# Kernel optimization log

Measured on AMD Instinct MI355X. Metric: run time of the kernel, lower is better.

The kernel has to match this reference:

```python
import jax, jax.numpy as jnp
import numpy as np

T_, N_, DIN, D, HEADS, WW, E_, DPE = 8, 20000, 128, 128, 4, 4, 320000, 8
DH = D // HEADS
NEG = -1e30
EPS_GATE = 1e-6


def setup_inputs() -> dict:
    key = jax.random.key(0)
    ks = jax.random.split(key, 10)
    return {
        "H_tilde": jax.random.normal(ks[0], (T_, N_, DIN), jnp.float32),
        "S": jax.random.uniform(ks[1], (T_, N_), jnp.float32),
        "Wq": jax.random.normal(ks[2], (D, DIN), jnp.float32) * 0.05,
        "Wkh": jax.random.normal(ks[3], (D, DIN), jnp.float32) * 0.05,
        "Wkpe": jax.random.normal(ks[4], (D, DPE), jnp.float32) * 0.05,
        "Wv": jax.random.normal(ks[5], (D, DIN), jnp.float32) * 0.05,
        "pe_table": jax.random.normal(ks[6], (WW + 1, DPE), jnp.float32),
        "rel_bias": jax.random.normal(ks[7], (WW + 1,), jnp.float32),
        "src": jax.random.randint(ks[8], (E_,), 0, N_),
        "dst": jax.random.randint(ks[9], (E_,), 0, N_),
    }


def reference(H_tilde, S, Wq, Wkh, Wkpe, Wv, pe_table, rel_bias, src, dst):
    T, N, _ = H_tilde.shape
    H, dh, W = HEADS, DH, WW
    scale = dh ** -0.5
    dtype = H_tilde.dtype

    # Projections (torch Linear: x @ W.T). W_k over concat([H, pe]) splits additively.
    Q = (H_tilde @ Wq.T).reshape(T, N, H, dh)
    K0 = (H_tilde @ Wkh.T).reshape(T, N, H, dh)
    V = (H_tilde @ Wv.T).reshape(T, N, H, dh)
    pe_k = (pe_table @ Wkpe.T).reshape(W + 1, H, dh)
    gate = jnp.log(jnp.clip(S, 0.0, 1.0) + EPS_GATE)  # (T, N)

    # Pad W zero-steps in front so a length-(W+1) slice at t covers t-W..t.
    pad = lambda x: jnp.concatenate([jnp.zeros((W,) + x.shape[1:], x.dtype), x], axis=0)
    Kp, Vp, gp = pad(K0), pad(V), pad(gate)

    def step(_, tq):
        t, Qt = tq  # Qt: (N, H, dh)
        Kwin = jax.lax.dynamic_slice_in_dim(Kp, t, W + 1, 0)[::-1]  # (W+1,N,H,dh), dt=0..W
        Vwin = jax.lax.dynamic_slice_in_dim(Vp, t, W + 1, 0)[::-1]
        gwin = jax.lax.dynamic_slice_in_dim(gp, t, W + 1, 0)[::-1]  # (W+1, N)
        Qd = Qt[dst]  # (E, H, dh)

        scores = []
        for dt in range(W + 1):
            Ks = Kwin[dt][src] + pe_k[dt][None]  # (E, H, dh)
            s = (jnp.einsum('ehc,ehc->eh', Qd, Ks) * scale
                 + rel_bias[dt] + gwin[dt][src][:, None])
            scores.append(jnp.where(dt <= t, s, NEG))  # mask dt > t (W_eff = min(W, t))
        sc = jnp.stack(scores)  # (W+1, E, H)

        # Segment softmax over incoming edges of each dst node, jointly over dt.
        mx = jax.ops.segment_max(sc.transpose(1, 0, 2), dst, num_segments=N)  # (N,W+1,H)
        mx = mx.max(axis=1)  # (N, H)
        valid = (jnp.arange(W + 1) <= t)[:, None, None]
        ex = jnp.where(valid, jnp.exp(sc - mx[dst][None]), 0.0)  # (W+1, E, H)

        denom = jax.ops.segment_sum(ex.sum(axis=0), dst, num_segments=N)  # (N, H)
        numer = jnp.zeros((N, H, dh), dtype)
        for dt in range(W + 1):
            contrib = ex[dt][:, :, None] * Vwin[dt][src]  # (E, H, dh)
            numer = numer + jax.ops.segment_sum(contrib, dst, num_segments=N)

        msg = numer / jnp.maximum(denom, 1e-12)[:, :, None]  # (N, H, dh)
        return None, msg.reshape(N, H * dh)

    _, M_out = jax.lax.scan(step, None, (jnp.arange(T), Q))
    return M_out  # (T, N, d)
```

## Files before the change

kernel.cpp:

```cpp
#include <hip/hip_runtime.h>

typedef unsigned short u16;
typedef unsigned int u32;
typedef __attribute__((ext_vector_type(8))) __bf16 bf16x8;
typedef __attribute__((ext_vector_type(4))) float f32x4;
typedef __attribute__((ext_vector_type(4))) _Float16 f16x4;
typedef __attribute__((ext_vector_type(2))) unsigned u32x2;

constexpr int TT = 8, NN = 20000, DD = 128, EE = 320000;
constexpr int MAXDEG = 64;
constexpr float SCL = 0.17677669529663687f;
constexpr int VBLK2 = 544;

__device__ __forceinline__ u16 f2bf(float f) {
  return __builtin_bit_cast(u16, (__bf16)f);
}
__device__ __forceinline__ u16 f2h(float f) {
  return __builtin_bit_cast(u16, (_Float16)f);
}
__device__ __forceinline__ float blo(u32 u) { return __uint_as_float(u << 16); }
__device__ __forceinline__ float bhi(u32 u) { return __uint_as_float(u & 0xffff0000u); }

__device__ __forceinline__ bf16x8 cvt8(float4 f0, float4 f1) {
  bf16x8 r;
  r[0] = (__bf16)f0.x; r[1] = (__bf16)f0.y; r[2] = (__bf16)f0.z; r[3] = (__bf16)f0.w;
  r[4] = (__bf16)f1.x; r[5] = (__bf16)f1.y; r[6] = (__bf16)f1.z; r[7] = (__bf16)f1.w;
  return r;
}

__global__ void k_init(const float* __restrict__ pe_table, const float* __restrict__ Wkpe,
                       const float* __restrict__ Wq, const float* __restrict__ Wkh,
                       const float* __restrict__ Wv, const float* __restrict__ S,
                       float* __restrict__ pek, int* __restrict__ cnt,
                       u16* __restrict__ Wb, float* __restrict__ SgT) {
  int i = blockIdx.x * 256 + threadIdx.x;
  if (i < NN) cnt[i] = 0;
  if (i < 5 * DD) {
    int dt = i >> 7, j = i & 127;
    float s = 0.f;
    for (int p = 0; p < 8; ++p) s += pe_table[dt * 8 + p] * Wkpe[j * 8 + p];
    pek[i] = s;
  }
  if (i < 3 * DD * DD) {
    int y = i / (DD * DD), idx = i % (DD * DD);
    const float* W = (y == 0) ? Wq : (y == 1) ? Wkh : Wv;
    Wb[i] = f2bf(W[idx]);
  }
  if (i < TT * NN) {
    SgT[i] = fminf(fmaxf(S[i], 0.f), 1.f) + 1e-6f;
  }
}

__global__ void k_build(const int* __restrict__ src, const int* __restrict__ dst,
                        int* __restrict__ cnt, int* __restrict__ eslot) {
  int i = blockIdx.x * 256 + threadIdx.x;
  if (i < EE) {
    int d = dst[i];
    int p = atomicAdd(&cnt[d], 1);
    if (p < MAXDEG) eslot[d * MAXDEG + p] = src[i];
  }
}

__global__ __launch_bounds__(256) void k_proj6(
    const float* __restrict__ Hm, const u16* __restrict__ Wb,
    u16* __restrict__ Qb, u16* __restrict__ Kb, u16* __restrict__ Vb) {
  int tid = threadIdx.x;
  int lane = tid & 63, wv = tid >> 6;
  int wr = wv >> 1, wc = wv & 1;
  int l15 = lane & 15, lq = lane >> 4;
  size_t m0 = (size_t)blockIdx.x * 128;

  bf16x8 a[4][4];
#pragma unroll
  for (int ks = 0; ks < 4; ++ks) {
    int col0 = ks * 32 + lq * 8;
#pragma unroll
    for (int i = 0; i < 4; ++i) {
      const float* gp = Hm + (m0 + wr * 64 + i * 16 + l15) * DD + col0;
      a[ks][i] = cvt8(*(const float4*)gp, *(const float4*)(gp + 4));
    }
  }

  for (int y = 0; y < 3; ++y) {
    u16* Out = (y == 0) ? Qb : (y == 1) ? Kb : Vb;
    const bool asF16 = (y == 2);
    const u16* Wy = Wb + y * DD * DD;

    f32x4 acc[4][4];
    for (int i = 0; i < 4; ++i)
      for (int j = 0; j < 4; ++j) acc[i][j] = (f32x4){0.f, 0.f, 0.f, 0.f};

    for (int ks = 0; ks < 4; ++ks) {
      int col0 = ks * 32 + lq * 8;
      bf16x8 b[4];
#pragma unroll
      for (int j = 0; j < 4; ++j)
        b[j] = *(const bf16x8*)(Wy + (wc * 64 + j * 16 + l15) * DD + col0);
#pragma unroll
      for (int i = 0; i < 4; ++i)
#pragma unroll
        for (int j = 0; j < 4; ++j)
          acc[i][j] = __builtin_amdgcn_mfma_f32_16x16x32_bf16(a[ks][i], b[j], acc[i][j], 0, 0, 0);
    }

#pragma unroll
    for (int i = 0; i < 4; ++i)
#pragma unroll
      for (int j = 0; j < 4; ++j)
#pragma unroll
        for (int g = 0; g < 4; ++g) {
          size_t row = m0 + wr * 64 + i * 16 + lq * 4 + g;
          int col = wc * 64 + j * 16 + l15;
          Out[row * DD + col] = asF16 ? f2h(acc[i][j][g]) : f2bf(acc[i][j][g]);
        }
  }
}

__global__ __launch_bounds__(256, 8) void k_agg10(
    const u16* __restrict__ Qb, const u16* __restrict__ Kb, const u16* __restrict__ Vb,
    const float* __restrict__ SgT, const float* __restrict__ pek,
    const float* __restrict__ relb,
    const int* __restrict__ cnt, const int* __restrict__ eslot,
    float* __restrict__ outp) {
  __shared__ int srcS[MAXDEG];
  __shared__ float eS2[4][40];
  __shared__ u16 VldsS[4][VBLK2];
  int tid = threadIdx.x;
  const int h = tid >> 6, lane = tid & 63;
  const int n = blockIdx.x;

  int deg = min(cnt[n], MAXDEG);
  if (tid < MAXDEG) srcS[tid] = (tid < deg) ? eslot[n * MAXDEG + tid] : 0;

  const int t16 = lane & 15, qo = lane >> 4, qo4 = qo * 4;
  const int h32 = h * 32;

  uint4 qb;
  {
    bool qok = t16 < 8;
    const u16* Qp = Qb + ((size_t)(t16 & 7) * NN + n) * DD + h32 + qo * 8;
    qb = qok ? *(const uint4*)(Qp) : make_uint4(0u, 0u, 0u, 0u);
  }

  {
    float qf0 = blo(qb.x), qf1 = bhi(qb.x), qf2 = blo(qb.y), qf3 = bhi(qb.y);
    float qf4 = blo(qb.z), qf5 = bhi(qb.z), qf6 = blo(qb.w), qf7 = bhi(qb.w);
#pragma unroll
    for (int d = 0; d < 5; ++d) {
      const float* pp = pek + d * DD + h32 + qo * 8;
      float4 p0 = *(const float4*)pp;
      float4 p1 = *(const float4*)(pp + 4);
      float s = qf0 * p0.x + qf1 * p0.y + qf2 * p0.z + qf3 * p0.w
              + qf4 * p1.x + qf5 * p1.y + qf6 * p1.z + qf7 * p1.w;
      s += __shfl_xor(s, 16);
      s += __shfl_xor(s, 32);
      if (qo == 0 && t16 < 8) eS2[h][t16 * 5 + d] = __expf(s * SCL + relb[d]);
    }
  }
  __syncthreads();

  f32x4 num0 = (f32x4){0.f, 0.f, 0.f, 0.f};
  f32x4 num1 = (f32x4){0.f, 0.f, 0.f, 0.f};
  float dd = 0.f;

  if (deg > 0) {
    const int degm1 = deg - 1;
    const int nch = (deg + 15) >> 4;
    const int cmax = nch << 4;
    const int nj = nch * 8;

    const int vkey = lane >> 2, vcb = lane & 3;
    u16* vbuf = &VldsS[h][0];
    unsigned trbase = (unsigned)(uintptr_t)vbuf + lane * 8;
    unsigned woff = (unsigned)((vcb >> 1) * VBLK2 + (vkey >> 2) * 128 +
                               (vkey & 3) * 32 + (vcb & 1) * 16);

    auto loadK = [&](int tp, int c16) -> uint4 {
      return *(const uint4*)(Kb + (size_t)tp * (NN * DD)
                             + (size_t)srcS[min(c16 + t16, degm1)] * DD + h32 + qo * 8);
    };
    auto loadV = [&](int tp, int c16) -> uint4 {
      return *(const uint4*)(Vb + (size_t)tp * (NN * DD)
                             + (size_t)srcS[min(c16 + vkey, degm1)] * DD + h32 + vcb * 8);
    };
    auto loadSg = [&](int tp, int c16) -> float {
      return SgT[(size_t)tp * NN + srcS[min(c16 + t16, degm1)]];
    };
    auto writeV = [&](uint4 f) { *(uint4*)((char*)vbuf + woff) = f; };
    auto compute = [&](uint4 ka, float sg, int tp, int c16) {
      int dt = t16 - tp;
      bool tval = (dt >= 0) && (dt <= 4) && (t16 < 8);
      float Ef = tval ? eS2[h][t16 * 5 + dt] : 0.f;

      f32x4 z = (f32x4){0.f, 0.f, 0.f, 0.f};
      f32x4 sc = __builtin_amdgcn_mfma_f32_16x16x32_bf16(
          __builtin_bit_cast(bf16x8, ka), __builtin_bit_cast(bf16x8, qb), z, 0, 0, 0);

      f16x4 wf;
      float w0, w1, w2, w3;
      {
        float g0 = __shfl(sg, qo4 + 0), g1 = __shfl(sg, qo4 + 1);
        float g2 = __shfl(sg, qo4 + 2), g3 = __shfl(sg, qo4 + 3);
        g0 = ((c16 + qo4 + 0) < deg) ? g0 : 0.f;
        g1 = ((c16 + qo4 + 1) < deg) ? g1 : 0.f;
        g2 = ((c16 + qo4 + 2) < deg) ? g2 : 0.f;
        g3 = ((c16 + qo4 + 3) < deg) ? g3 : 0.f;
        w0 = __expf(sc[0] * SCL) * Ef * g0;
        w1 = __expf(sc[1] * SCL) * Ef * g1;
        w2 = __expf(sc[2] * SCL) * Ef * g2;
        w3 = __expf(sc[3] * SCL) * Ef * g3;
      }
      dd += w0 + w1 + w2 + w3;
      wf[0] = (_Float16)w0; wf[1] = (_Float16)w1;
      wf[2] = (_Float16)w2; wf[3] = (_Float16)w3;

      __builtin_amdgcn_sched_barrier(0);
      u32x2 vr0, vr1;
      asm volatile("ds_read_b64_tr_b16 %0, %1" : "=v"(vr0) : "v"(trbase));
      asm volatile("ds_read_b64_tr_b16 %0, %1 offset:544" : "=v"(vr1) : "v"(trbase));
      asm volatile("s_waitcnt lgkmcnt(0)");
      __builtin_amdgcn_sched_barrier(0);
      num0 = __builtin_amdgcn_mfma_f32_16x16x16f16(
          wf, __builtin_bit_cast(f16x4, vr0), num0, 0, 0, 0);
      num1 = __builtin_amdgcn_mfma_f32_16x16x16f16(
          wf, __builtin_bit_cast(f16x4, vr1), num1, 0, 0, 0);
    };

    uint4 kA = loadK(0, 0);
    float sgA = loadSg(0, 0);
    writeV(loadV(0, 0));
    int tpj = 0, cj = 0;
    int tpn = 0, cn = 16;
    if (cn >= cmax) { cn = 0; tpn = 1; }

    for (int j = 0; j < nj; ++j) {
      bool more = (j + 1) < nj;
      uint4 kB = make_uint4(0u, 0u, 0u, 0u), vB = make_uint4(0u, 0u, 0u, 0u);
      float sgB = 0.f;
      if (more) {
        kB = loadK(tpn, cn);
        vB = loadV(tpn, cn);
        sgB = loadSg(tpn, cn);
      }
      compute(kA, sgA, tpj, cj);
      __builtin_amdgcn_sched_barrier(0);
      if (more) writeV(vB);
      kA = kB;
      sgA = sgB;
      tpj = tpn; cj = cn;
      cn += 16;
      if (cn >= cmax) { cn = 0; ++tpn; }
    }
  }

  float Dh = dd;
  Dh += __shfl_xor(Dh, 16);
  Dh += __shfl_xor(Dh, 32);
#pragma unroll
  for (int r = 0; r < 4; ++r) {
    int t = qo4 + r;
    float Dt = __shfl(Dh, t);
    if (t < 8) {
      float inv = 1.f / fmaxf(Dt, 1e-12f);
      float* op = outp + ((size_t)t * NN + n) * DD + h32;
      op[t16] = num0[r] * inv;
      op[16 + t16] = num1[r] * inv;
    }
  }
}

extern "C" void kernel_launch(void* const* d_in, const int* in_sizes, int n_in,
                              void* d_out, int out_size, void* d_ws, size_t ws_size,
                              hipStream_t stream) {
  const float* Hm = (const float*)d_in[0];
  const float* S = (const float*)d_in[1];
  const float* Wq = (const float*)d_in[2];
  const float* Wkh = (const float*)d_in[3];
  const float* Wkpe = (const float*)d_in[4];
  const float* Wv = (const float*)d_in[5];
  const float* pe_table = (const float*)d_in[6];
  const float* relb = (const float*)d_in[7];
  const int* src = (const int*)d_in[8];
  const int* dst = (const int*)d_in[9];
  float* out = (float*)d_out;

  auto aup = [](size_t x) { return (x + 255) & ~(size_t)255; };
  char* base = (char*)d_ws;
  size_t off = 0;
  u16* Qb = (u16*)(base + off); off = aup(off + (size_t)TT * NN * DD * 2);
  u16* Kb = (u16*)(base + off); off = aup(off + (size_t)TT * NN * DD * 2);
  u16* Vb = (u16*)(base + off); off = aup(off + (size_t)TT * NN * DD * 2);
  float* pek = (float*)(base + off); off = aup(off + (size_t)5 * DD * 4);
  float* SgT = (float*)(base + off); off = aup(off + (size_t)TT * NN * 4);
  int* cnt = (int*)(base + off); off = aup(off + (size_t)NN * 4);
  int* eslot = (int*)(base + off); off = aup(off + (size_t)NN * MAXDEG * 4);
  u16* Wb = (u16*)(base + off); off = aup(off + (size_t)3 * DD * DD * 2);
  (void)ws_size; (void)in_sizes; (void)n_in; (void)out_size;

  k_init<<<(TT * NN + 255) / 256, 256, 0, stream>>>(pe_table, Wkpe, Wq, Wkh, Wv, S,
                                                    pek, cnt, Wb, SgT);
  k_build<<<(EE + 255) / 256, 256, 0, stream>>>(src, dst, cnt, eslot);
  k_proj6<<<1250, 256, 0, stream>>>(Hm, Wb, Qb, Kb, Vb);
  k_agg10<<<NN, 256, 0, stream>>>(Qb, Kb, Vb, SgT, pek, relb, cnt, eslot, out);
}
```

Measured before the change: 309.4 us.

## Fold softmax scale into Q projection and stage gate values in LDS

```diff
diff --git a/kernel.cpp b/kernel.cpp
--- a/kernel.cpp
+++ b/kernel.cpp
@@ -84,6 +84,7 @@
   for (int y = 0; y < 3; ++y) {
     u16* Out = (y == 0) ? Qb : (y == 1) ? Kb : Vb;
     const bool asF16 = (y == 2);
+    const float postm = (y == 0) ? SCL : 1.f;
     const u16* Wy = Wb + y * DD * DD;
 
     f32x4 acc[4][4];
@@ -111,26 +112,37 @@
         for (int g = 0; g < 4; ++g) {
           size_t row = m0 + wr * 64 + i * 16 + lq * 4 + g;
           int col = wc * 64 + j * 16 + l15;
-          Out[row * DD + col] = asF16 ? f2h(acc[i][j][g]) : f2bf(acc[i][j][g]);
+          float v = acc[i][j][g] * postm;
+          Out[row * DD + col] = asF16 ? f2h(v) : f2bf(v);
         }
   }
 }
 
-__global__ __launch_bounds__(256, 8) void k_agg10(
+__global__ __launch_bounds__(256, 8) void k_agg11(
     const u16* __restrict__ Qb, const u16* __restrict__ Kb, const u16* __restrict__ Vb,
     const float* __restrict__ SgT, const float* __restrict__ pek,
     const float* __restrict__ relb,
     const int* __restrict__ cnt, const int* __restrict__ eslot,
     float* __restrict__ outp) {
-  __shared__ int srcS[MAXDEG];
-  __shared__ float eS2[4][40];
+  __shared__ int srcB[MAXDEG];
+  __shared__ float gateS[TT][MAXDEG];
+  __shared__ float eW[4][TT][16];
   __shared__ u16 VldsS[4][VBLK2];
   int tid = threadIdx.x;
   const int h = tid >> 6, lane = tid & 63;
   const int n = blockIdx.x;
 
   int deg = min(cnt[n], MAXDEG);
-  if (tid < MAXDEG) srcS[tid] = (tid < deg) ? eslot[n * MAXDEG + tid] : 0;
+  if (tid < MAXDEG) {
+    int s = (tid < deg) ? eslot[n * MAXDEG + tid] : 0;
+    srcB[tid] = s * DD;
+  }
+  for (int i = tid; i < TT * MAXDEG; i += 256) {
+    int tp = i >> 6, e = i & 63;
+    float g = 0.f;
+    if (e < deg) g = SgT[(size_t)tp * NN + eslot[n * MAXDEG + e]];
+    gateS[tp][e] = g;
+  }
 
   const int t16 = lane & 15, qo = lane >> 4, qo4 = qo * 4;
   const int h32 = h * 32;
@@ -143,6 +155,8 @@
   }
 
   {
+    ((float*)&eW[h][0][0])[lane] = -1e30f;
+    ((float*)&eW[h][0][0])[lane + 64] = -1e30f;
     float qf0 = blo(qb.x), qf1 = bhi(qb.x), qf2 = blo(qb.y), qf3 = bhi(qb.y);
     float qf4 = blo(qb.z), qf5 = bhi(qb.z), qf6 = blo(qb.w), qf7 = bhi(qb.w);
 #pragma unroll
@@ -154,7 +168,8 @@
               + qf4 * p1.x + qf5 * p1.y + qf6 * p1.z + qf7 * p1.w;
       s += __shfl_xor(s, 16);
       s += __shfl_xor(s, 32);
-      if (qo == 0 && t16 < 8) eS2[h][t16 * 5 + d] = __expf(s * SCL + relb[d]);
+      int tp = t16 - d;
+      if (qo == 0 && t16 < 8 && tp >= 0) eW[h][tp][t16] = s + relb[d];
     }
   }
   __syncthreads();
@@ -174,43 +189,33 @@
     unsigned trbase = (unsigned)(uintptr_t)vbuf + lane * 8;
     unsigned woff = (unsigned)((vcb >> 1) * VBLK2 + (vkey >> 2) * 128 +
                                (vkey & 3) * 32 + (vcb & 1) * 16);
+    const float* eWt = &eW[h][0][t16];
 
     auto loadK = [&](int tp, int c16) -> uint4 {
       return *(const uint4*)(Kb + (size_t)tp * (NN * DD)
-                             + (size_t)srcS[min(c16 + t16, degm1)] * DD + h32 + qo * 8);
+                             + (size_t)srcB[min(c16 + t16, degm1)] + h32 + qo * 8);
     };
     auto loadV = [&](int tp, int c16) -> uint4 {
       return *(const uint4*)(Vb + (size_t)tp * (NN * DD)
-                             + (size_t)srcS[min(c16 + vkey, degm1)] * DD + h32 + vcb * 8);
+                             + (size_t)srcB[min(c16 + vkey, degm1)] + h32 + vcb * 8);
     };
-    auto loadSg = [&](int tp, int c16) -> float {
-      return SgT[(size_t)tp * NN + srcS[min(c16 + t16, degm1)]];
+    auto loadG = [&](int tp, int c16) -> f32x4 {
+      return *(const f32x4*)&gateS[tp][c16 + qo4];
     };
     auto writeV = [&](uint4 f) { *(uint4*)((char*)vbuf + woff) = f; };
-    auto compute = [&](uint4 ka, float sg, int tp, int c16) {
-      int dt = t16 - tp;
-      bool tval = (dt >= 0) && (dt <= 4) && (t16 < 8);
-      float Ef = tval ? eS2[h][t16 * 5 + dt] : 0.f;
+    auto compute = [&](uint4 ka, f32x4 g4, int tp) {
+      float Lf = eWt[tp * 16];
 
       f32x4 z = (f32x4){0.f, 0.f, 0.f, 0.f};
       f32x4 sc = __builtin_amdgcn_mfma_f32_16x16x32_bf16(
           __builtin_bit_cast(bf16x8, ka), __builtin_bit_cast(bf16x8, qb), z, 0, 0, 0);
 
+      float w0 = __expf(sc[0] + Lf) * g4[0];
+      float w1 = __expf(sc[1] + Lf) * g4[1];
+      float w2 = __expf(sc[2] + Lf) * g4[2];
+      float w3 = __expf(sc[3] + Lf) * g4[3];
+      dd += w0 + w1 + w2 + w3;
       f16x4 wf;
-      float w0, w1, w2, w3;
-      {
-        float g0 = __shfl(sg, qo4 + 0), g1 = __shfl(sg, qo4 + 1);
-        float g2 = __shfl(sg, qo4 + 2), g3 = __shfl(sg, qo4 + 3);
-        g0 = ((c16 + qo4 + 0) < deg) ? g0 : 0.f;
-        g1 = ((c16 + qo4 + 1) < deg) ? g1 : 0.f;
-        g2 = ((c16 + qo4 + 2) < deg) ? g2 : 0.f;
-        g3 = ((c16 + qo4 + 3) < deg) ? g3 : 0.f;
-        w0 = __expf(sc[0] * SCL) * Ef * g0;
-        w1 = __expf(sc[1] * SCL) * Ef * g1;
-        w2 = __expf(sc[2] * SCL) * Ef * g2;
-        w3 = __expf(sc[3] * SCL) * Ef * g3;
-      }
-      dd += w0 + w1 + w2 + w3;
       wf[0] = (_Float16)w0; wf[1] = (_Float16)w1;
       wf[2] = (_Float16)w2; wf[3] = (_Float16)w3;
 
@@ -227,27 +232,27 @@
     };
 
     uint4 kA = loadK(0, 0);
-    float sgA = loadSg(0, 0);
+    f32x4 gA = loadG(0, 0);
     writeV(loadV(0, 0));
-    int tpj = 0, cj = 0;
+    int tpj = 0;
     int tpn = 0, cn = 16;
     if (cn >= cmax) { cn = 0; tpn = 1; }
 
     for (int j = 0; j < nj; ++j) {
       bool more = (j + 1) < nj;
       uint4 kB = make_uint4(0u, 0u, 0u, 0u), vB = make_uint4(0u, 0u, 0u, 0u);
-      float sgB = 0.f;
+      f32x4 gB = (f32x4){0.f, 0.f, 0.f, 0.f};
       if (more) {
         kB = loadK(tpn, cn);
         vB = loadV(tpn, cn);
-        sgB = loadSg(tpn, cn);
+        gB = loadG(tpn, cn);
       }
-      compute(kA, sgA, tpj, cj);
+      compute(kA, gA, tpj);
       __builtin_amdgcn_sched_barrier(0);
       if (more) writeV(vB);
       kA = kB;
-      sgA = sgB;
-      tpj = tpn; cj = cn;
+      gA = gB;
+      tpj = tpn;
       cn += 16;
       if (cn >= cmax) { cn = 0; ++tpn; }
     }
@@ -301,5 +306,5 @@
                                                     pek, cnt, Wb, SgT);
   k_build<<<(EE + 255) / 256, 256, 0, stream>>>(src, dst, cnt, eslot);
   k_proj6<<<1250, 256, 0, stream>>>(Hm, Wb, Qb, Kb, Vb);
-  k_agg10<<<NN, 256, 0, stream>>>(Qb, Kb, Vb, SgT, pek, relb, cnt, eslot, out);
-}
+  k_agg11<<<NN, 256, 0, stream>>>(Qb, Kb, Vb, SgT, pek, relb, cnt, eslot, out);
+}
```

Measured after the change: 302.1 us. -2.4%, faster.
